# Kernel tuning notes

Hardware: AMD Instinct MI355X
Metric: run time of the kernel (lower is better)

The kernel has to match this reference:

```python
import jax, jax.numpy as jnp
import numpy as np

B, S, D, H = 2, 2048, 1024, 16
DK = D // H  # 64
THETA = 10000.0
SCALE = 1.0 / np.sqrt(DK)


def _rope(t, pos):
    """Apply rotary embedding. t: [b,h,s,dk], pos: [b,s] int."""
    inv_freq = THETA ** (-jnp.arange(0, DK, 2, dtype=jnp.float32) / DK)  # [dk/2]
    ang = pos[:, None, :, None].astype(jnp.float32) * inv_freq  # [b,1,s,dk/2]
    cos, sin = jnp.cos(ang), jnp.sin(ang)
    t1, t2 = t[..., 0::2], t[..., 1::2]  # interleaved pairs
    rot = jnp.stack([t1 * cos - t2 * sin, t1 * sin + t2 * cos], axis=-1)
    return rot.reshape(t.shape)


def setup_inputs() -> dict:
    key = jax.random.key(0)
    ks = jax.random.split(key, 9)
    sc = 0.02
    x = jax.random.normal(ks[0], (B, S, D), jnp.float32)
    token_position = jnp.tile(jnp.arange(S, dtype=jnp.int32)[None, :], (B, 1))
    Wq = jax.random.normal(ks[1], (D, D), jnp.float32) * sc
    Wk = jax.random.normal(ks[2], (D, D), jnp.float32) * sc
    Wv = jax.random.normal(ks[3], (D, D), jnp.float32) * sc
    Wo = jax.random.normal(ks[4], (D, D), jnp.float32) * sc
    bq = jnp.zeros((D,), jnp.float32)
    bk = jnp.zeros((D,), jnp.float32)
    bv = jnp.zeros((D,), jnp.float32)
    bo = jnp.zeros((D,), jnp.float32)
    return {"x": x, "token_position": token_position,
            "Wq": Wq, "bq": bq, "Wk": Wk, "bk": bk,
            "Wv": Wv, "bv": bv, "Wo": Wo, "bo": bo}


def reference(x, token_position, Wq, bq, Wk, bk, Wv, bv, Wo, bo):
    b, s, d = x.shape
    # projections, split heads: [b,s,d] -> [b,h,s,dk]
    def heads(t):
        return t.reshape(b, s, H, DK).transpose(0, 2, 1, 3)
    q = heads(x @ Wq + bq)
    k = heads(x @ Wk + bk)
    v = heads(x @ Wv + bv)
    q = _rope(q, token_position)
    k = _rope(k, token_position)
    scores = jnp.einsum('bhnk,bhmk->bhnm', q, k) * SCALE  # [b,h,s,s]
    causal = jnp.tril(jnp.ones((s, s), dtype=bool))
    scores = jnp.where(causal, scores, -jnp.inf)
    probs = jax.nn.softmax(scores, axis=-1)
    o = jnp.einsum('bhnm,bhmk->bhnk', probs, v)  # [b,h,s,dk]
    o = o.transpose(0, 2, 1, 3).reshape(b, s, d)
    return o @ Wo + bo
```

## Files before the change

kernel.cpp:

```cpp
#include <hip/hip_runtime.h>
#include <math.h>

#define BB  2
#define SS  2048
#define DD  1024
#define HH  16
#define DKK 64

constexpr float kScale = 0.125f;
constexpr float kC1 = 0.18033688011112042f;
constexpr float kC2 = 23.0831206542234144f;

typedef __bf16 bf16x8 __attribute__((ext_vector_type(8)));
typedef __bf16 bf16x4 __attribute__((ext_vector_type(4)));
typedef float f32x4 __attribute__((ext_vector_type(4)));

__device__ __forceinline__ void async_copy16(const void* g, void* l) {
  __builtin_amdgcn_global_load_lds(
      (const __attribute__((address_space(1))) void*)g,
      (__attribute__((address_space(3))) void*)l, 16, 0, 0);
}

__global__ __launch_bounds__(256) void prep_kernel(
    const float* __restrict__ x, const int* __restrict__ pos,
    const float* __restrict__ W0, const float* __restrict__ W1,
    const float* __restrict__ W2, const float* __restrict__ W3,
    __bf16* __restrict__ xb, float2* __restrict__ rtab,
    __bf16* __restrict__ T0, __bf16* __restrict__ T1,
    __bf16* __restrict__ T2, __bf16* __restrict__ T3) {
  __shared__ __bf16 tile[64][65];
  const int bid = blockIdx.x;
  const int t = threadIdx.x;
  if (bid < 2048) {
    const size_t i = ((size_t)bid * 256 + t) * 8;
    const float4 v0 = *(const float4*)(x + i);
    const float4 v1 = *(const float4*)(x + i + 4);
    bf16x8 o;
    o[0] = (__bf16)v0.x; o[1] = (__bf16)v0.y; o[2] = (__bf16)v0.z; o[3] = (__bf16)v0.w;
    o[4] = (__bf16)v1.x; o[5] = (__bf16)v1.y; o[6] = (__bf16)v1.z; o[7] = (__bf16)v1.w;
    *(bf16x8*)(xb + i) = o;
  } else if (bid < 2560) {
    const int idx = (bid - 2048) * 256 + t;
    const int m = idx >> 5, pi = idx & 31;
    const float inv = exp2f(-0.4152410118609203f * (float)pi);
    float sn, cs;
    __sincosf((float)pos[m] * inv, &sn, &cs);
    rtab[idx] = make_float2(cs, sn);
  } else {
    const int tid2 = bid - 2560;
    const int z = tid2 >> 8, rem = tid2 & 255;
    const float* W;
    __bf16* T;
    switch (z) {
      case 0: W = W0; T = T0; break;
      case 1: W = W1; T = T1; break;
      case 2: W = W2; T = T2; break;
      default: W = W3; T = T3; break;
    }
    const int k0 = (rem >> 4) * 64, n0 = (rem & 15) * 64;
    const int c = t & 63, rg = t >> 6;
#pragma unroll
    for (int i = 0; i < 16; i++) {
      const int r = rg + i * 4;
      tile[r][c] = (__bf16)W[(size_t)(k0 + r) * DD + n0 + c];
    }
    __syncthreads();
#pragma unroll
    for (int i = 0; i < 16; i++) {
      const int r = rg + i * 4;
      T[(size_t)(n0 + r) * DD + k0 + c] = tile[c][r];
    }
  }
}

__device__ __forceinline__ void gemm_core(
    const __bf16* __restrict__ A, const __bf16* __restrict__ Bt,
    int bm, int bn, f32x4 (&acc)[4][4], __bf16* As, __bf16* Bs) {
  const int t = threadIdx.x;
  const int lane = t & 63, wave = t >> 6;
  const int col = lane & 15, quad = lane >> 4;
  const int wm = (wave & 1) * 64, wn = (wave >> 1) * 64;
  const int r8 = lane >> 3;
  const int cg = (lane & 7) ^ r8;
  const __bf16* ag = A + (size_t)(bm + wave * 32 + r8) * DD + cg * 8;
  const __bf16* bg = Bt + (size_t)(bn + wave * 32 + r8) * DD + cg * 8;
  __bf16* asb = As + wave * 32 * 64;
  __bf16* bsb = Bs + wave * 32 * 64;

  for (int kt = 0; kt < DD; kt += 64) {
#pragma unroll
    for (int c = 0; c < 4; c++) {
      async_copy16(ag + (size_t)c * 8 * DD + kt, asb + c * 512);
      async_copy16(bg + (size_t)c * 8 * DD + kt, bsb + c * 512);
    }
    __syncthreads();
#pragma unroll
    for (int ks = 0; ks < 2; ks++) {
      bf16x8 af[4], bf[4];
#pragma unroll
      for (int i = 0; i < 4; i++)
        af[i] = *(const bf16x8*)(As + (wm + i * 16 + col) * 64 +
                                 (((ks * 4 + quad) ^ (col & 7)) * 8));
#pragma unroll
      for (int j = 0; j < 4; j++)
        bf[j] = *(const bf16x8*)(Bs + (wn + j * 16 + col) * 64 +
                                 (((ks * 4 + quad) ^ (col & 7)) * 8));
#pragma unroll
      for (int i = 0; i < 4; i++)
#pragma unroll
        for (int j = 0; j < 4; j++)
          acc[i][j] =
              __builtin_amdgcn_mfma_f32_16x16x32_bf16(af[i], bf[j], acc[i][j], 0, 0, 0);
    }
    __syncthreads();
  }
}

__global__ __launch_bounds__(256) void qkv_gemm_kernel(
    const __bf16* __restrict__ xb, const __bf16* __restrict__ WqT,
    const __bf16* __restrict__ WkT, const __bf16* __restrict__ WvT,
    const float* __restrict__ bq, const float* __restrict__ bk,
    const float* __restrict__ bv, const float2* __restrict__ ropetab,
    __bf16* __restrict__ qo, __bf16* __restrict__ ko, __bf16* __restrict__ vo) {
  __shared__ __bf16 As[128 * 64];
  __shared__ __bf16 Bs[128 * 64];
  const int mat = blockIdx.x >> 3;
  const int bn = (blockIdx.x & 7) * 128;
  const int bm = blockIdx.y * 128;

  f32x4 acc[4][4] = {};
  const int t = threadIdx.x, lane = t & 63, wave = t >> 6;
  const int col = lane & 15, quad = lane >> 4;
  const int wm = (wave & 1) * 64, wn = (wave >> 1) * 64;

  if (mat == 2) {
    gemm_core(WvT, xb, bn, bm, acc, As, Bs);
    const int b = bm >> 11;
#pragma unroll
    for (int i = 0; i < 4; i++) {
#pragma unroll
      for (int r = 0; r < 4; r++) {
        const int n = bn + wm + i * 16 + quad * 4 + r;
        const float bb = bv[n];
        const int h = n >> 6, dk = n & 63;
        __bf16* vrow = vo + ((size_t)(b * HH + h) * DKK + dk) * SS;
#pragma unroll
        for (int j = 0; j < 4; j++) {
          const int m = bm + wn + j * 16 + col;
          vrow[m & (SS - 1)] = (__bf16)(acc[i][j][r] + bb);
        }
      }
    }
    return;
  }

  const __bf16* Bt = mat == 0 ? WqT : WkT;
  const float* bias = mat == 0 ? bq : bk;
  __bf16* out = mat == 0 ? qo : ko;
  gemm_core(xb, Bt, bm, bn, acc, As, Bs);

#pragma unroll
  for (int i = 0; i < 4; i++) {
#pragma unroll
    for (int j = 0; j < 4; j++) {
      const int n = bn + wn + j * 16 + col;
      const float bb = bias[n];
      const int pi = (n & 63) >> 1;
#pragma unroll
      for (int r = 0; r < 4; r++) {
        const int m = bm + wm + i * 16 + quad * 4 + r;
        float v = acc[i][j][r] + bb;
        {
          const float other = __shfl_xor(v, 1, 64);
          const float2 cssn = ropetab[(size_t)m * 32 + pi];
          v = (n & 1) ? (other * cssn.y + v * cssn.x)
                      : (v * cssn.x - other * cssn.y);
        }
        const int h = n >> 6, dk = n & 63;
        const int b = m >> 11, s = m & (SS - 1);
        out[((size_t)(b * HH + h) * SS + s) * DKK + dk] = (__bf16)v;
      }
    }
  }
}

__global__ __launch_bounds__(256) void oproj_gemm_kernel(
    const __bf16* __restrict__ ob, const __bf16* __restrict__ WoT,
    const float* __restrict__ bo, float* __restrict__ out) {
  __shared__ __bf16 As[128 * 64];
  __shared__ __bf16 Bs[128 * 64];
  const int bn = blockIdx.x * 128;
  const int bm = blockIdx.y * 128;
  f32x4 acc[4][4] = {};
  gemm_core(ob, WoT, bm, bn, acc, As, Bs);

  const int t = threadIdx.x, lane = t & 63, wave = t >> 6;
  const int col = lane & 15, quad = lane >> 4;
  const int wm = (wave & 1) * 64, wn = (wave >> 1) * 64;
#pragma unroll
  for (int i = 0; i < 4; i++) {
#pragma unroll
    for (int j = 0; j < 4; j++) {
      const int n = bn + wn + j * 16 + col;
      const float bb = bo[n];
#pragma unroll
      for (int r = 0; r < 4; r++) {
        const int m = bm + wm + i * 16 + quad * 4 + r;
        out[(size_t)m * DD + n] = acc[i][j][r] + bb;
      }
    }
  }
}

template <bool kMask>
__device__ __forceinline__ void attn_tile(
    const __bf16* __restrict__ Kbuf, const __bf16* __restrict__ Vbuf,
    __bf16* __restrict__ pw, const bf16x8 (&qf)[2][2], f32x4 (&oacc)[2][4],
    float (&l_lane)[2], int tok0, int rbase_w, int col, int quad) {
  bf16x8 kf[4][2];
#pragma unroll
  for (int ct = 0; ct < 4; ct++)
#pragma unroll
    for (int ks = 0; ks < 2; ks++)
      kf[ct][ks] = *(const bf16x8*)(Kbuf + (ct * 16 + col) * 64 +
                                    (((ks * 4 + quad) ^ (col & 7)) * 8));
#pragma unroll
  for (int rt = 0; rt < 2; rt++) {
    f32x4 sc[4] = {};
#pragma unroll
    for (int ct = 0; ct < 4; ct++)
#pragma unroll
      for (int ks = 0; ks < 2; ks++)
        sc[ct] = __builtin_amdgcn_mfma_f32_16x16x32_bf16(kf[ct][ks],
                                                         qf[rt][ks], sc[ct],
                                                         0, 0, 0);
    const int rg = rbase_w + rt * 16 + col;
#pragma unroll
    for (int ct = 0; ct < 4; ct++) {
      bf16x4 pk;
#pragma unroll
      for (int r = 0; r < 4; r++) {
        float p = exp2f(sc[ct][r] * kC1 - kC2);
        if (kMask && (tok0 + ct * 16 + quad * 4 + r) > rg) p = 0.0f;
        l_lane[rt] += p;
        pk[r] = (__bf16)p;
      }
      *(bf16x4*)(pw + (rt * 16 + col) * 72 + ct * 16 + quad * 4) = pk;
    }
  }
  bf16x8 vf[4][2];
#pragma unroll
  for (int dt = 0; dt < 4; dt++)
#pragma unroll
    for (int ks = 0; ks < 2; ks++)
      vf[dt][ks] = *(const bf16x8*)(Vbuf + (dt * 16 + col) * 64 +
                                    (((ks * 4 + quad) ^ (col & 7)) * 8));
#pragma unroll
  for (int rt = 0; rt < 2; rt++) {
    bf16x8 pf[2];
#pragma unroll
    for (int ks = 0; ks < 2; ks++)
      pf[ks] =
          *(const bf16x8*)(pw + (rt * 16 + col) * 72 + ks * 32 + quad * 8);
#pragma unroll
    for (int dt = 0; dt < 4; dt++)
#pragma unroll
      for (int ks = 0; ks < 2; ks++)
        oacc[rt][dt] = __builtin_amdgcn_mfma_f32_16x16x32_bf16(
            pf[ks], vf[dt][ks], oacc[rt][dt], 0, 0, 0);
  }
}

__global__ __launch_bounds__(256) void flash_attn_mfma_kernel(
    const __bf16* __restrict__ q, const __bf16* __restrict__ k,
    const __bf16* __restrict__ vt, __bf16* __restrict__ o) {
  __shared__ __bf16 Ks[2][64 * 64];
  __shared__ __bf16 Vs[2][64 * 64];
  __shared__ __bf16 Ps[4][32 * 72];

  const int bh = blockIdx.x;
  const int pr = blockIdx.y;
  const int t = threadIdx.x, lane = t & 63, wave = t >> 6;
  const int col = lane & 15, quad = lane >> 4;
  const int r8 = lane >> 3;
  const int cg = (lane & 7) ^ r8;

  const __bf16* qb = q + (size_t)bh * SS * DKK;
  const __bf16* kb = k + (size_t)bh * SS * DKK;
  const __bf16* vtb = vt + (size_t)bh * DKK * SS;
  const int b = bh / HH, h = bh % HH;
  __bf16* pw = (__bf16*)Ps[wave];

#pragma unroll
  for (int phase = 0; phase < 2; phase++) {
    const int qt = phase == 0 ? pr : (15 - pr);
    const int rbase_w = qt * 128 + wave * 32;

    bf16x8 qf[2][2];
#pragma unroll
    for (int rt = 0; rt < 2; rt++)
#pragma unroll
      for (int ks = 0; ks < 2; ks++)
        qf[rt][ks] = *(const bf16x8*)(qb +
                                      (size_t)(rbase_w + rt * 16 + col) * DKK +
                                      ks * 32 + quad * 8);

    f32x4 oacc[2][4] = {};
    float l_lane[2] = {0.f, 0.f};

    const int nkt = 2 * qt + 2;

#pragma unroll
    for (int i = 0; i < 2; i++) {
      const int slab = wave * 2 + i;
      async_copy16(kb + (size_t)(slab * 8 + r8) * DKK + cg * 8,
                   Ks[0] + slab * 512);
      async_copy16(vtb + (size_t)(slab * 8 + r8) * SS + cg * 8,
                   Vs[0] + slab * 512);
    }

    for (int kt = 0; kt < nkt; kt++) {
      const int cur = kt & 1;
      __syncthreads();

      if (kt + 1 < nkt) {
#pragma unroll
        for (int i = 0; i < 2; i++) {
          const int slab = wave * 2 + i;
          async_copy16(
              kb + (size_t)((kt + 1) * 64 + slab * 8 + r8) * DKK + cg * 8,
              Ks[cur ^ 1] + slab * 512);
          async_copy16(
              vtb + (size_t)(slab * 8 + r8) * SS + (kt + 1) * 64 + cg * 8,
              Vs[cur ^ 1] + slab * 512);
        }
      }

      const int tok0 = kt * 64;
      if (tok0 <= rbase_w + 31) {
        if (tok0 + 63 <= rbase_w)
          attn_tile<false>(Ks[cur], Vs[cur], pw, qf, oacc, l_lane, tok0,
                           rbase_w, col, quad);
        else
          attn_tile<true>(Ks[cur], Vs[cur], pw, qf, oacc, l_lane, tok0,
                          rbase_w, col, quad);
      }
    }
    __syncthreads();

#pragma unroll
    for (int rt = 0; rt < 2; rt++) {
      float l = l_lane[rt];
      l += __shfl_xor(l, 16, 64);
      l += __shfl_xor(l, 32, 64);
#pragma unroll
      for (int r = 0; r < 4; r++) {
        const float lr = __shfl(l, quad * 4 + r, 64);
        const float inv_l = 1.0f / lr;
        const int s = rbase_w + rt * 16 + quad * 4 + r;
#pragma unroll
        for (int dt = 0; dt < 4; dt++)
          o[((size_t)(b * SS + s) * HH + h) * DKK + dt * 16 + col] =
              (__bf16)(oacc[rt][dt][r] * inv_l);
      }
    }
  }
}

extern "C" void kernel_launch(void* const* d_in, const int* in_sizes, int n_in,
                              void* d_out, int out_size, void* d_ws,
                              size_t ws_size, hipStream_t stream) {
  const float* x  = (const float*)d_in[0];
  const int*  pos = (const int*)d_in[1];
  const float* Wq = (const float*)d_in[2];
  const float* bq = (const float*)d_in[3];
  const float* Wk = (const float*)d_in[4];
  const float* bk = (const float*)d_in[5];
  const float* Wv = (const float*)d_in[6];
  const float* bv = (const float*)d_in[7];
  const float* Wo = (const float*)d_in[8];
  const float* bo = (const float*)d_in[9];
  float* out = (float*)d_out;

  char* ws = (char*)d_ws;
  __bf16* xb  = (__bf16*)(ws);
  __bf16* WqT = (__bf16*)(ws + ((size_t)8  << 20));
  __bf16* WkT = (__bf16*)(ws + ((size_t)10 << 20));
  __bf16* WvT = (__bf16*)(ws + ((size_t)12 << 20));
  __bf16* WoT = (__bf16*)(ws + ((size_t)14 << 20));
  __bf16* qb  = (__bf16*)(ws + ((size_t)16 << 20));
  __bf16* kb  = (__bf16*)(ws + ((size_t)24 << 20));
  __bf16* vtb = (__bf16*)(ws + ((size_t)32 << 20));
  __bf16* ob  = (__bf16*)(ws + ((size_t)40 << 20));
  float2* rtab = (float2*)(ws + ((size_t)48 << 20));

  prep_kernel<<<3584, 256, 0, stream>>>(x, pos, Wq, Wk, Wv, Wo, xb, rtab, WqT,
                                        WkT, WvT, WoT);
  qkv_gemm_kernel<<<dim3(24, 32), 256, 0, stream>>>(xb, WqT, WkT, WvT, bq, bk,
                                                    bv, rtab, qb, kb, vtb);
  flash_attn_mfma_kernel<<<dim3(32, 8), 256, 0, stream>>>(qb, kb, vtb, ob);
  oproj_gemm_kernel<<<dim3(8, 32), 256, 0, stream>>>(ob, WoT, bo, out);
}
```

Before: 212.1 us.

## Read K/V fragments directly from global memory and remap attention grid per XCD

The attention kernel no longer stages K and V tiles in LDS with async copies and block barriers. Each wave now loads its K and V MFMA fragments straight from global memory, relying on L2/cache reuse. The grid becomes 512 one-dimensional blocks with independent per-wave query strips, mapped so that heads group by XCD and longest strips are scheduled first. This removes syncthreads and LDS traffic but adds redundant global loads per wave and uncoalesced strided V reads.

Result: slower. 241.4 us (+13.8%).

```diff
diff --git a/kernel.cpp b/kernel.cpp
--- a/kernel.cpp
+++ b/kernel.cpp
@@ -214,16 +214,23 @@
 
 template <bool kMask>
 __device__ __forceinline__ void attn_tile(
-    const __bf16* __restrict__ Kbuf, const __bf16* __restrict__ Vbuf,
+    const __bf16* __restrict__ kg, const __bf16* __restrict__ vg,
     __bf16* __restrict__ pw, const bf16x8 (&qf)[2][2], f32x4 (&oacc)[2][4],
     float (&l_lane)[2], int tok0, int rbase_w, int col, int quad) {
-  bf16x8 kf[4][2];
+  bf16x8 kf[4][2], vf[4][2];
 #pragma unroll
   for (int ct = 0; ct < 4; ct++)
 #pragma unroll
     for (int ks = 0; ks < 2; ks++)
-      kf[ct][ks] = *(const bf16x8*)(Kbuf + (ct * 16 + col) * 64 +
-                                    (((ks * 4 + quad) ^ (col & 7)) * 8));
+      kf[ct][ks] = *(const bf16x8*)(kg + (ct * 16 + col) * 64 + ks * 32 +
+                                    quad * 8);
+#pragma unroll
+  for (int dt = 0; dt < 4; dt++)
+#pragma unroll
+    for (int ks = 0; ks < 2; ks++)
+      vf[dt][ks] = *(const bf16x8*)(vg + (size_t)(dt * 16 + col) * SS +
+                                    ks * 32 + quad * 8);
+
 #pragma unroll
   for (int rt = 0; rt < 2; rt++) {
     f32x4 sc[4] = {};
@@ -248,13 +255,6 @@
       *(bf16x4*)(pw + (rt * 16 + col) * 72 + ct * 16 + quad * 4) = pk;
     }
   }
-  bf16x8 vf[4][2];
-#pragma unroll
-  for (int dt = 0; dt < 4; dt++)
-#pragma unroll
-    for (int ks = 0; ks < 2; ks++)
-      vf[dt][ks] = *(const bf16x8*)(Vbuf + (dt * 16 + col) * 64 +
-                                    (((ks * 4 + quad) ^ (col & 7)) * 8));
 #pragma unroll
   for (int rt = 0; rt < 2; rt++) {
     bf16x8 pf[2];
@@ -274,16 +274,16 @@
 __global__ __launch_bounds__(256) void flash_attn_mfma_kernel(
     const __bf16* __restrict__ q, const __bf16* __restrict__ k,
     const __bf16* __restrict__ vt, __bf16* __restrict__ o) {
-  __shared__ __bf16 Ks[2][64 * 64];
-  __shared__ __bf16 Vs[2][64 * 64];
   __shared__ __bf16 Ps[4][32 * 72];
 
-  const int bh = blockIdx.x;
-  const int pr = blockIdx.y;
+  const int u = blockIdx.x;
+  const int xcd = u & 7;
+  const int i = u >> 3;
+  const int bh = xcd * 4 + (i & 3);
+  const int j = i >> 2;
   const int t = threadIdx.x, lane = t & 63, wave = t >> 6;
   const int col = lane & 15, quad = lane >> 4;
-  const int r8 = lane >> 3;
-  const int cg = (lane & 7) ^ r8;
+  const int s = 63 - (j * 4 + wave);
 
   const __bf16* qb = q + (size_t)bh * SS * DKK;
   const __bf16* kb = k + (size_t)bh * SS * DKK;
@@ -291,78 +291,41 @@
   const int b = bh / HH, h = bh % HH;
   __bf16* pw = (__bf16*)Ps[wave];
 
-#pragma unroll
-  for (int phase = 0; phase < 2; phase++) {
-    const int qt = phase == 0 ? pr : (15 - pr);
-    const int rbase_w = qt * 128 + wave * 32;
-
-    bf16x8 qf[2][2];
-#pragma unroll
-    for (int rt = 0; rt < 2; rt++)
-#pragma unroll
-      for (int ks = 0; ks < 2; ks++)
-        qf[rt][ks] = *(const bf16x8*)(qb +
-                                      (size_t)(rbase_w + rt * 16 + col) * DKK +
-                                      ks * 32 + quad * 8);
-
-    f32x4 oacc[2][4] = {};
-    float l_lane[2] = {0.f, 0.f};
-
-    const int nkt = 2 * qt + 2;
-
-#pragma unroll
-    for (int i = 0; i < 2; i++) {
-      const int slab = wave * 2 + i;
-      async_copy16(kb + (size_t)(slab * 8 + r8) * DKK + cg * 8,
-                   Ks[0] + slab * 512);
-      async_copy16(vtb + (size_t)(slab * 8 + r8) * SS + cg * 8,
-                   Vs[0] + slab * 512);
-    }
-
-    for (int kt = 0; kt < nkt; kt++) {
-      const int cur = kt & 1;
-      __syncthreads();
-
-      if (kt + 1 < nkt) {
-#pragma unroll
-        for (int i = 0; i < 2; i++) {
-          const int slab = wave * 2 + i;
-          async_copy16(
-              kb + (size_t)((kt + 1) * 64 + slab * 8 + r8) * DKK + cg * 8,
-              Ks[cur ^ 1] + slab * 512);
-          async_copy16(
-              vtb + (size_t)(slab * 8 + r8) * SS + (kt + 1) * 64 + cg * 8,
-              Vs[cur ^ 1] + slab * 512);
-        }
-      }
-
-      const int tok0 = kt * 64;
-      if (tok0 <= rbase_w + 31) {
-        if (tok0 + 63 <= rbase_w)
-          attn_tile<false>(Ks[cur], Vs[cur], pw, qf, oacc, l_lane, tok0,
-                           rbase_w, col, quad);
-        else
-          attn_tile<true>(Ks[cur], Vs[cur], pw, qf, oacc, l_lane, tok0,
-                          rbase_w, col, quad);
-      }
-    }
-    __syncthreads();
-
-#pragma unroll
-    for (int rt = 0; rt < 2; rt++) {
-      float l = l_lane[rt];
-      l += __shfl_xor(l, 16, 64);
-      l += __shfl_xor(l, 32, 64);
-#pragma unroll
-      for (int r = 0; r < 4; r++) {
-        const float lr = __shfl(l, quad * 4 + r, 64);
-        const float inv_l = 1.0f / lr;
-        const int s = rbase_w + rt * 16 + quad * 4 + r;
-#pragma unroll
-        for (int dt = 0; dt < 4; dt++)
-          o[((size_t)(b * SS + s) * HH + h) * DKK + dt * 16 + col] =
-              (__bf16)(oacc[rt][dt][r] * inv_l);
-      }
+  const int rbase_w = s * 32;
+
+  bf16x8 qf[2][2];
+#pragma unroll
+  for (int rt = 0; rt < 2; rt++)
+#pragma unroll
+    for (int ks = 0; ks < 2; ks++)
+      qf[rt][ks] = *(const bf16x8*)(qb +
+                                    (size_t)(rbase_w + rt * 16 + col) * DKK +
+                                    ks * 32 + quad * 8);
+
+  f32x4 oacc[2][4] = {};
+  float l_lane[2] = {0.f, 0.f};
+
+  const int kdiag = s >> 1;
+  for (int kt = 0; kt < kdiag; kt++)
+    attn_tile<false>(kb + (size_t)kt * 64 * DKK, vtb + kt * 64, pw, qf, oacc,
+                     l_lane, kt * 64, rbase_w, col, quad);
+  attn_tile<true>(kb + (size_t)kdiag * 64 * DKK, vtb + kdiag * 64, pw, qf,
+                  oacc, l_lane, kdiag * 64, rbase_w, col, quad);
+
+#pragma unroll
+  for (int rt = 0; rt < 2; rt++) {
+    float l = l_lane[rt];
+    l += __shfl_xor(l, 16, 64);
+    l += __shfl_xor(l, 32, 64);
+#pragma unroll
+    for (int r = 0; r < 4; r++) {
+      const float lr = __shfl(l, quad * 4 + r, 64);
+      const float inv_l = 1.0f / lr;
+      const int srow = rbase_w + rt * 16 + quad * 4 + r;
+#pragma unroll
+      for (int dt = 0; dt < 4; dt++)
+        o[((size_t)(b * SS + srow) * HH + h) * DKK + dt * 16 + col] =
+            (__bf16)(oacc[rt][dt][r] * inv_l);
     }
   }
 }
@@ -398,6 +361,6 @@
                                         WkT, WvT, WoT);
   qkv_gemm_kernel<<<dim3(24, 32), 256, 0, stream>>>(xb, WqT, WkT, WvT, bq, bk,
                                                     bv, rtab, qb, kb, vtb);
-  flash_attn_mfma_kernel<<<dim3(32, 8), 256, 0, stream>>>(qb, kb, vtb, ob);
+  flash_attn_mfma_kernel<<<512, 256, 0, stream>>>(qb, kb, vtb, ob);
   oproj_gemm_kernel<<<dim3(8, 32), 256, 0, stream>>>(ob, WoT, bo, out);
 }
```
